# Performance work log

Hardware: AMD Instinct MI355X
Metric: run time of the kernel (lower is better)

## Reference

```python
import jax, jax.numpy as jnp
import numpy as np

N, E, G = 50000, 500000, 8
IN, HID, OUT, NC, H = 256, 128, 64, 10, 2
NPG = N // G  # nodes per graph
NEG_SLOPE = 0.2


def setup_inputs() -> dict:
    key = jax.random.key(0)
    ks = jax.random.split(key, 24)
    x = jax.random.normal(ks[0], (N, IN), jnp.float32)
    # edges constrained to stay within each graph, no self-loops
    src = jax.random.randint(ks[1], (E,), 0, N)
    base = (src // NPG) * NPG
    off = jax.random.randint(ks[2], (E,), 1, NPG)
    dst = base + (src - base + off) % NPG
    edge_index = jnp.stack([src, dst], axis=0).astype(jnp.int32)
    edge_attr = jax.random.uniform(ks[3], (E, 1), jnp.float32)
    batch = jnp.repeat(jnp.arange(G, dtype=jnp.int32), NPG)
    y = jax.random.randint(ks[4], (N,), 0, NC).astype(jnp.int32)

    s = 0.1
    p = {
        'W1': jax.random.normal(ks[5], (IN, H * HID), jnp.float32) * s,
        'att_src1': jax.random.normal(ks[6], (H, HID), jnp.float32) * s,
        'att_dst1': jax.random.normal(ks[7], (H, HID), jnp.float32) * s,
        'We1': jax.random.normal(ks[8], (1, H * HID), jnp.float32) * s,
        'att_edge1': jax.random.normal(ks[9], (H, HID), jnp.float32) * s,
        'b1': jnp.zeros((HID,), jnp.float32),
        'W2': jax.random.normal(ks[10], (HID, H * OUT), jnp.float32) * s,
        'att_src2': jax.random.normal(ks[11], (H, OUT), jnp.float32) * s,
        'att_dst2': jax.random.normal(ks[12], (H, OUT), jnp.float32) * s,
        'We2': jax.random.normal(ks[13], (1, H * OUT), jnp.float32) * s,
        'att_edge2': jax.random.normal(ks[14], (H, OUT), jnp.float32) * s,
        'b2': jnp.zeros((OUT,), jnp.float32),
        'Wc': jax.random.normal(ks[15], (OUT, NC), jnp.float32) * s,
        'bc': jnp.zeros((NC,), jnp.float32),
    }
    return dict(x=x, edge_index=edge_index, edge_attr=edge_attr, batch=batch, y=y, **p)


def _gat_layer(x, src, dst, eattr, W, a_src, a_dst, We, a_e, b, n_nodes, C):
    # PyG GATConv: heads=H, concat=False (mean over heads), edge_dim features.
    xp = (x @ W).reshape(n_nodes, H, C)                    # [N,H,C]
    al_s = jnp.einsum('nhc,hc->nh', xp, a_src)             # [N,H]
    al_d = jnp.einsum('nhc,hc->nh', xp, a_dst)
    ef = (eattr @ We).reshape(-1, H, C)                    # [E,H,C]
    al_e = jnp.einsum('ehc,hc->eh', ef, a_e)               # [E,H]
    alpha = jax.nn.leaky_relu(al_s[src] + al_d[dst] + al_e, NEG_SLOPE)
    # edge softmax grouped by destination (every dst has a self-loop -> no empty segs)
    m = jax.ops.segment_max(alpha, dst, num_segments=n_nodes)
    ex = jnp.exp(alpha - m[dst])
    denom = jax.ops.segment_sum(ex, dst, num_segments=n_nodes)
    w = ex / (denom[dst] + 1e-16)                          # [E,H]
    msg = xp[src] * w[:, :, None]                          # [E,H,C]
    out = jax.ops.segment_sum(msg, dst, num_segments=n_nodes)  # [N,H,C]
    return out.mean(axis=1) + b


def reference(x, edge_index, edge_attr, batch, y,
              W1, att_src1, att_dst1, We1, att_edge1, b1,
              W2, att_src2, att_dst2, We2, att_edge2, b2,
              Wc, bc):
    src, dst = edge_index[0], edge_index[1]
    # add self-loops; edge_attr fill = per-graph mean (as in the per-graph loop)
    g = batch[src]
    cnt = jax.ops.segment_sum(jnp.ones_like(edge_attr[:, 0]), g, num_segments=G)
    mean_attr = jax.ops.segment_sum(edge_attr, g, num_segments=G) / cnt[:, None]
    loop_attr = mean_attr[batch]                           # [N,1]
    ar = jnp.arange(N, dtype=src.dtype)
    src_a = jnp.concatenate([src, ar])
    dst_a = jnp.concatenate([dst, ar])
    ea = jnp.concatenate([edge_attr, loop_attr], axis=0)

    h = _gat_layer(x, src_a, dst_a, ea, W1, att_src1, att_dst1, We1, att_edge1, b1, N, HID)
    h = jax.nn.relu(h)
    h = _gat_layer(h, src_a, dst_a, ea, W2, att_src2, att_dst2, We2, att_edge2, b2, N, OUT)
    pred = h @ Wc + bc                                     # [N,NC]
    return pred, y
```

## Files before the change

kernel.cpp:

```cpp
#include <hip/hip_runtime.h>
#include <hip/hip_bf16.h>
#include <cstdint>
#include <cstddef>

#define N_NODES 50000
#define N_EDGES 500000
#define EA_EDGES 550000
#define NPG 6250
#define G_GRAPHS 8
#define IN_DIM 256
#define HID_DIM 128
#define OUT_DIM 64
#define NCLS 10
#define NEG_SLOPE 0.2f
#define M_PAD 50048

typedef __attribute__((ext_vector_type(8))) short short8v;
typedef __attribute__((ext_vector_type(4))) float f32x4;

__device__ __forceinline__ unsigned short f2bf(float f) {
  __hip_bfloat16 h = __float2bfloat16(f);
  unsigned short u;
  __builtin_memcpy(&u, &h, 2);
  return u;
}
__device__ __forceinline__ float bf2f(unsigned short u) {
  return __uint_as_float(((unsigned)u) << 16);
}

__device__ __forceinline__ void gl_lds16(const unsigned short* g, unsigned short* l) {
  __builtin_amdgcn_global_load_lds(
      (const __attribute__((address_space(1))) unsigned int*)(g),
      (__attribute__((address_space(3))) unsigned int*)(l),
      16, 0, 0);
}

__global__ void k_sums_degree(const int* __restrict__ src, const int* __restrict__ dst,
                              const float* __restrict__ eattr,
                              float* __restrict__ sums, float* __restrict__ cnts,
                              int* __restrict__ deg) {
  __shared__ float ls[G_GRAPHS], lc[G_GRAPHS];
  if (threadIdx.x < G_GRAPHS) { ls[threadIdx.x] = 0.f; lc[threadIdx.x] = 0.f; }
  __syncthreads();
  int stride = gridDim.x * blockDim.x;
  for (int e = blockIdx.x * blockDim.x + threadIdx.x; e < EA_EDGES; e += stride) {
    if (e < N_EDGES) {
      int g = src[e] / NPG;
      atomicAdd(&ls[g], eattr[e]);
      atomicAdd(&lc[g], 1.f);
      atomicAdd(&deg[dst[e]], 1);
    } else {
      atomicAdd(&deg[e - N_EDGES], 1);
    }
  }
  __syncthreads();
  if (threadIdx.x < G_GRAPHS) {
    atomicAdd(&sums[threadIdx.x], ls[threadIdx.x]);
    atomicAdd(&cnts[threadIdx.x], lc[threadIdx.x]);
  }
}

__global__ void k_prep(const float* __restrict__ sums, const float* __restrict__ cnts,
                       float* __restrict__ mean,
                       const float* __restrict__ We1, const float* __restrict__ ae1,
                       const float* __restrict__ We2, const float* __restrict__ ae2,
                       float* __restrict__ ce) {
  if (threadIdx.x == 0 && blockIdx.x == 0) {
    for (int g = 0; g < G_GRAPHS; ++g) mean[g] = sums[g] / cnts[g];
    for (int h = 0; h < 2; ++h) {
      float s = 0.f;
      for (int c = 0; c < HID_DIM; ++c) s += We1[h * HID_DIM + c] * ae1[h * HID_DIM + c];
      ce[h] = s;
    }
    for (int h = 0; h < 2; ++h) {
      float s = 0.f;
      for (int c = 0; c < OUT_DIM; ++c) s += We2[h * OUT_DIM + c] * ae2[h * OUT_DIM + c];
      ce[2 + h] = s;
    }
  }
}

__global__ void k_scan1(const int* __restrict__ deg, int* __restrict__ rowptr,
                        int* __restrict__ bsum, int n) {
  __shared__ int sm[1024];
  int tid = threadIdx.x;
  int i = blockIdx.x * 1024 + tid;
  int v = (i < n) ? deg[i] : 0;
  sm[tid] = v;
  __syncthreads();
  for (int off = 1; off < 1024; off <<= 1) {
    int t = (tid >= off) ? sm[tid - off] : 0;
    __syncthreads();
    if (tid >= off) sm[tid] += t;
    __syncthreads();
  }
  if (i < n) rowptr[i] = sm[tid] - v;
  if (tid == 1023) bsum[blockIdx.x] = sm[1023];
}

__global__ void k_scan2(int* __restrict__ bsum, int* __restrict__ rowptr, int nb, int n) {
  if (threadIdx.x == 0 && blockIdx.x == 0) {
    int run = 0;
    for (int i = 0; i < nb; ++i) { int v = bsum[i]; bsum[i] = run; run += v; }
    rowptr[n] = run;
  }
}

__global__ void k_scan3(int* __restrict__ rowptr, int* __restrict__ cursor,
                        const int* __restrict__ bsum, int n) {
  int i = blockIdx.x * blockDim.x + threadIdx.x;
  if (i < n) {
    int r = rowptr[i] + bsum[i >> 10];
    rowptr[i] = r;
    cursor[i] = r;
  }
}

__global__ void k_fill(const int* __restrict__ src, const int* __restrict__ dst,
                       const float* __restrict__ eattr, const float* __restrict__ mean,
                       int* __restrict__ cursor, int2* __restrict__ csr) {
  int e = blockIdx.x * blockDim.x + threadIdx.x;
  if (e >= EA_EDGES) return;
  int s, d; float a;
  if (e < N_EDGES) { s = src[e]; d = dst[e]; a = eattr[e]; }
  else { int i = e - N_EDGES; s = i; d = i; a = mean[i / NPG]; }
  int p = atomicAdd(&cursor[d], 1);
  csr[p] = make_int2(s, __float_as_int(a));
}

__global__ void k_cast_bf16(const float* __restrict__ in, unsigned short* __restrict__ out, int n8) {
  int i = blockIdx.x * blockDim.x + threadIdx.x;
  if (i >= n8) return;
  float4 a = *(const float4*)(in + (size_t)i * 8);
  float4 b = *(const float4*)(in + (size_t)i * 8 + 4);
  uint4 o;
  o.x = (unsigned)f2bf(a.x) | ((unsigned)f2bf(a.y) << 16);
  o.y = (unsigned)f2bf(a.z) | ((unsigned)f2bf(a.w) << 16);
  o.z = (unsigned)f2bf(b.x) | ((unsigned)f2bf(b.y) << 16);
  o.w = (unsigned)f2bf(b.z) | ((unsigned)f2bf(b.w) << 16);
  *(uint4*)(out + (size_t)i * 8) = o;
}

__global__ void k_cast_t(const float* __restrict__ W, unsigned short* __restrict__ Wt,
                         int K, int N) {
  int i = blockIdx.x * blockDim.x + threadIdx.x;
  if (i >= K * N) return;
  int k = i / N, n = i - k * N;
  Wt[(size_t)n * K + k] = f2bf(W[i]);
}

template <int K>
__global__ __launch_bounds__(256) void k_gemm_mfma(const unsigned short* __restrict__ A,
                                                   const unsigned short* __restrict__ Bt,
                                                   unsigned short* __restrict__ C,
                                                   int M, int Nout,
                                                   const float* __restrict__ a_src,
                                                   const float* __restrict__ a_dst,
                                                   float* __restrict__ als,
                                                   float* __restrict__ ald) {
  constexpr int BM = 128, BN = 128, BK = 64;
  constexpr int TSZ = BM * BK;
  __shared__ __attribute__((aligned(16))) unsigned short As[2 * TSZ];
  __shared__ __attribute__((aligned(16))) unsigned short Bs[2 * TSZ];
  const int tid = threadIdx.x;
  const int lane = tid & 63;
  const int wid = tid >> 6;
  const int wr = wid >> 1, wc = wid & 1;
  const int r0 = blockIdx.y * BM, c0 = blockIdx.x * BN;
  f32x4 acc[4][4] = {};

  const int srow = wid * 32 + (lane >> 3);
  const int schunk = (lane & 7) ^ (lane >> 3);
  const unsigned short* gA = A + (size_t)(r0 + srow) * K + schunk * 8;
  const unsigned short* gB = Bt + (size_t)(c0 + srow) * K + schunk * 8;

  auto stage = [&](int buf, int k0) {
    unsigned short* Ab = As + buf * TSZ + wid * 2048;
    unsigned short* Bb = Bs + buf * TSZ + wid * 2048;
#pragma unroll
    for (int i = 0; i < 4; ++i) {
      gl_lds16(gA + (size_t)(i * 8) * K + k0, Ab + i * 512);
      gl_lds16(gB + (size_t)(i * 8) * K + k0, Bb + i * 512);
    }
  };

  constexpr int NT = K / BK;
  int cur = 0;
  stage(0, 0);
#pragma unroll
  for (int t = 0; t < NT; ++t) {
    __syncthreads();
    if (t + 1 < NT) stage(cur ^ 1, (t + 1) * BK);
    const char* Ab = (const char*)(As + cur * TSZ);
    const char* Bb = (const char*)(Bs + cur * TSZ);
#pragma unroll
    for (int ks = 0; ks < 2; ++ks) {
      short8v a[4], b[4];
#pragma unroll
      for (int mi = 0; mi < 4; ++mi) {
        int row = wr * 64 + mi * 16 + (lane & 15);
        int boff = (row * 128 + ks * 64 + (lane >> 4) * 16) ^ ((row & 7) << 4);
        a[mi] = *(const short8v*)(Ab + boff);
      }
#pragma unroll
      for (int ni = 0; ni < 4; ++ni) {
        int row = wc * 64 + ni * 16 + (lane & 15);
        int boff = (row * 128 + ks * 64 + (lane >> 4) * 16) ^ ((row & 7) << 4);
        b[ni] = *(const short8v*)(Bb + boff);
      }
#pragma unroll
      for (int mi = 0; mi < 4; ++mi)
#pragma unroll
        for (int ni = 0; ni < 4; ++ni)
          acc[mi][ni] = __builtin_amdgcn_mfma_f32_16x16x32_bf16(a[mi], b[ni], acc[mi][ni], 0, 0, 0);
    }
    cur ^= 1;
  }

#pragma unroll
  for (int mi = 0; mi < 4; ++mi) {
#pragma unroll
    for (int r = 0; r < 4; ++r) {
      int row = r0 + wr * 64 + mi * 16 + (lane >> 4) * 4 + r;
      if (row < M) {
#pragma unroll
        for (int ni = 0; ni < 4; ++ni) {
          int col = c0 + wc * 64 + ni * 16 + (lane & 15);
          C[(size_t)row * Nout + col] = f2bf(acc[mi][ni][r]);
        }
      }
    }
  }

  {
    int headc = (c0 + wc * 64) / (Nout >> 1);
    float asv[4], adv[4];
#pragma unroll
    for (int ni = 0; ni < 4; ++ni) {
      int col = c0 + wc * 64 + ni * 16 + (lane & 15);
      asv[ni] = a_src[col];
      adv[ni] = a_dst[col];
    }
#pragma unroll
    for (int mi = 0; mi < 4; ++mi) {
#pragma unroll
      for (int r = 0; r < 4; ++r) {
        float ps = 0.f, pd = 0.f;
#pragma unroll
        for (int ni = 0; ni < 4; ++ni) {
          ps += acc[mi][ni][r] * asv[ni];
          pd += acc[mi][ni][r] * adv[ni];
        }
#pragma unroll
        for (int off = 1; off < 16; off <<= 1) {
          ps += __shfl_xor(ps, off);
          pd += __shfl_xor(pd, off);
        }
        int row = r0 + wr * 64 + mi * 16 + (lane >> 4) * 4 + r;
        if ((lane & 15) == 0 && row < M) {
          atomicAdd(&als[2 * row + headc], ps);
          atomicAdd(&ald[2 * row + headc], pd);
        }
      }
    }
  }
}

template <int C, bool RELU, bool BF16OUT>
__global__ void k_aggregate(const unsigned short* __restrict__ xp,
                            const float* __restrict__ als, const float* __restrict__ ald,
                            const int* __restrict__ rowptr, const int2* __restrict__ csr,
                            const float* __restrict__ ce,
                            const float* __restrict__ bias, void* __restrict__ outv) {
  constexpr int TC = 2 * C;
  constexpr int VPL = TC / 64;
  int lane = threadIdx.x & 63;
  int wid = threadIdx.x >> 6;
  int local = (blockIdx.x >> 3) * 4 + wid;
  if (local >= NPG) return;
  int node = (blockIdx.x & 7) * NPG + local;
  int p0 = rowptr[node], p1 = rowptr[node + 1];
  int deg = p1 - p0;
  int half = lane >> 5;
  int sub = lane & 31;
  float ald_m = ald[2 * node + half];
  float ce_m = ce[half];
  float m = -1e30f, den = 0.f;
  float acc[VPL];
#pragma unroll
  for (int k = 0; k < VPL; ++k) acc[k] = 0.f;

  for (int base = 0; base < deg; base += 32) {
    int nE = min(32, deg - base);
    float a = -1e30f;
    int s = 0;
    float w = 0.f;
    if (sub < nE) {
      int2 md = csr[p0 + base + sub];
      s = md.x;
      float ea = __int_as_float(md.y);
      float l = als[2 * s + half] + ald_m + ce_m * ea;
      a = (l > 0.f) ? l : NEG_SLOPE * l;
    }
    float cm = a;
#pragma unroll
    for (int off = 1; off < 32; off <<= 1) cm = fmaxf(cm, __shfl_xor(cm, off));
    float nm = fmaxf(m, cm);
    float cs = __expf(m - nm);
    m = nm;
    if (sub < nE) w = __expf(a - m);
    float ws = w;
#pragma unroll
    for (int off = 1; off < 32; off <<= 1) ws += __shfl_xor(ws, off);
    den = den * cs + ws;
#pragma unroll
    for (int k = 0; k < VPL; ++k) acc[k] *= cs;
    for (int e0 = 0; e0 < nE; e0 += 8) {
      int se[8]; float wh[8];
#pragma unroll
      for (int j = 0; j < 8; ++j) {
        int e = e0 + j;
        se[j] = __shfl(s, e);
        wh[j] = __shfl(w, e | (lane & 32));
      }
      if (VPL == 4) {
        ushort4 u[8];
#pragma unroll
        for (int j = 0; j < 8; ++j)
          u[j] = *(const ushort4*)(xp + (size_t)se[j] * TC + lane * VPL);
#pragma unroll
        for (int j = 0; j < 8; ++j) {
          acc[0] += wh[j] * bf2f(u[j].x);
          acc[1] += wh[j] * bf2f(u[j].y);
          acc[2] += wh[j] * bf2f(u[j].z);
          acc[3] += wh[j] * bf2f(u[j].w);
        }
      } else {
        ushort2 u[8];
#pragma unroll
        for (int j = 0; j < 8; ++j)
          u[j] = *(const ushort2*)(xp + (size_t)se[j] * TC + lane * VPL);
#pragma unroll
        for (int j = 0; j < 8; ++j) {
          acc[0] += wh[j] * bf2f(u[j].x);
          acc[1] += wh[j] * bf2f(u[j].y);
        }
      }
    }
  }

  float deni = 1.f / (den + 1e-16f);
  float t[VPL];
#pragma unroll
  for (int k = 0; k < VPL; ++k) {
    t[k] = acc[k] * deni;
    t[k] += __shfl_xor(t[k], 32);
  }
  if (lane < 32) {
    int c = lane * VPL;
    float v[VPL];
#pragma unroll
    for (int k = 0; k < VPL; ++k) {
      v[k] = 0.5f * t[k] + bias[c + k];
      if (RELU) v[k] = fmaxf(v[k], 0.f);
    }
    if (BF16OUT) {
      unsigned short* o = (unsigned short*)outv + (size_t)node * C + c;
      if (VPL == 4) {
        ushort4 u;
        u.x = f2bf(v[0]); u.y = f2bf(v[1]); u.z = f2bf(v[2]); u.w = f2bf(v[3]);
        *(ushort4*)o = u;
      } else {
        ushort2 u; u.x = f2bf(v[0]); u.y = f2bf(v[1]);
        *(ushort2*)o = u;
      }
    } else {
      float* o = (float*)outv + (size_t)node * C + c;
#pragma unroll
      for (int k = 0; k < VPL; ++k) o[k] = v[k];
    }
  }
}

__global__ void k_classifier(const float* __restrict__ h2, const float* __restrict__ Wc,
                             const float* __restrict__ bc, const int* __restrict__ y,
                             float* __restrict__ out) {
  __shared__ float wcs[OUT_DIM * NCLS];
  __shared__ float bcs[NCLS];
  for (int i = threadIdx.x; i < OUT_DIM * NCLS; i += blockDim.x) wcs[i] = Wc[i];
  if (threadIdx.x < NCLS) bcs[threadIdx.x] = bc[threadIdx.x];
  __syncthreads();
  int n = blockIdx.x * blockDim.x + threadIdx.x;
  if (n >= N_NODES) return;
  float acc[NCLS];
#pragma unroll
  for (int j = 0; j < NCLS; ++j) acc[j] = bcs[j];
  for (int k = 0; k < OUT_DIM; ++k) {
    float v = h2[(size_t)n * OUT_DIM + k];
#pragma unroll
    for (int j = 0; j < NCLS; ++j) acc[j] += v * wcs[k * NCLS + j];
  }
#pragma unroll
  for (int j = 0; j < NCLS; ++j) out[(size_t)n * NCLS + j] = acc[j];
  out[(size_t)N_NODES * NCLS + n] = (float)y[n];
}

extern "C" void kernel_launch(void* const* d_in, const int* in_sizes, int n_in,
                              void* d_out, int out_size, void* d_ws, size_t ws_size,
                              hipStream_t stream) {
  const float* x     = (const float*)d_in[0];
  const int*   ei    = (const int*)d_in[1];
  const float* eattr = (const float*)d_in[2];
  const int*   y     = (const int*)d_in[4];
  const float* W1  = (const float*)d_in[5];
  const float* as1 = (const float*)d_in[6];
  const float* ad1 = (const float*)d_in[7];
  const float* We1 = (const float*)d_in[8];
  const float* ae1 = (const float*)d_in[9];
  const float* b1  = (const float*)d_in[10];
  const float* W2  = (const float*)d_in[11];
  const float* as2 = (const float*)d_in[12];
  const float* ad2 = (const float*)d_in[13];
  const float* We2 = (const float*)d_in[14];
  const float* ae2 = (const float*)d_in[15];
  const float* b2  = (const float*)d_in[16];
  const float* Wc  = (const float*)d_in[17];
  const float* bc  = (const float*)d_in[18];
  float* out = (float*)d_out;

  const int* src = ei;
  const int* dst = ei + N_EDGES;

  char* wsb = (char*)d_ws;
  size_t o = 0;
  auto alloc = [&](size_t bytes) { size_t r = o; o = (o + bytes + 255) & ~(size_t)255; return r; };
  size_t o_sums   = alloc(G_GRAPHS * 4);
  size_t o_cnts   = alloc(G_GRAPHS * 4);
  size_t o_mean   = alloc(G_GRAPHS * 4);
  size_t o_ce     = alloc(4 * 4);
  size_t o_bsum   = alloc(64 * 4);
  size_t o_deg    = alloc((size_t)N_NODES * 4);
  size_t o_rowptr = alloc((size_t)(N_NODES + 1) * 4);
  size_t o_cursor = alloc((size_t)N_NODES * 4);
  size_t o_csr    = alloc((size_t)EA_EDGES * 8);
  size_t o_xb     = alloc((size_t)M_PAD * IN_DIM * 2);
  size_t o_wt1    = alloc((size_t)IN_DIM * 256 * 2);
  size_t o_wt2    = alloc((size_t)HID_DIM * 128 * 2);
  size_t o_xp     = alloc((size_t)N_NODES * 256 * 2);
  size_t o_h1b    = alloc((size_t)M_PAD * HID_DIM * 2);
  size_t o_h2     = alloc((size_t)N_NODES * OUT_DIM * 4);
  size_t o_als    = alloc((size_t)N_NODES * 2 * 4);
  size_t o_ald    = alloc((size_t)N_NODES * 2 * 4);
  (void)ws_size;

  float* sums   = (float*)(wsb + o_sums);
  float* cnts   = (float*)(wsb + o_cnts);
  float* mean   = (float*)(wsb + o_mean);
  float* ce     = (float*)(wsb + o_ce);
  int*   bsum   = (int*)(wsb + o_bsum);
  int*   deg    = (int*)(wsb + o_deg);
  int*   rowptr = (int*)(wsb + o_rowptr);
  int*   cursor = (int*)(wsb + o_cursor);
  int2*  csr    = (int2*)(wsb + o_csr);
  unsigned short* xb  = (unsigned short*)(wsb + o_xb);
  unsigned short* wt1 = (unsigned short*)(wsb + o_wt1);
  unsigned short* wt2 = (unsigned short*)(wsb + o_wt2);
  unsigned short* xp  = (unsigned short*)(wsb + o_xp);
  unsigned short* h1b = (unsigned short*)(wsb + o_h1b);
  float* h2     = (float*)(wsb + o_h2);
  float* als    = (float*)(wsb + o_als);
  float* ald    = (float*)(wsb + o_ald);
  size_t alsald_bytes = (o_ald - o_als) + (size_t)N_NODES * 2 * 4;

  hipMemsetAsync(sums, 0, G_GRAPHS * 4 * 2, stream);
  hipMemsetAsync(deg, 0, (size_t)N_NODES * 4, stream);

  k_cast_bf16<<<(N_NODES * IN_DIM / 8 + 255) / 256, 256, 0, stream>>>(x, xb, N_NODES * IN_DIM / 8);
  k_cast_t<<<(IN_DIM * 256 + 255) / 256, 256, 0, stream>>>(W1, wt1, IN_DIM, 256);
  k_cast_t<<<(HID_DIM * 128 + 255) / 256, 256, 0, stream>>>(W2, wt2, HID_DIM, 128);

  k_sums_degree<<<512, 256, 0, stream>>>(src, dst, eattr, sums, cnts, deg);
  k_prep<<<1, 64, 0, stream>>>(sums, cnts, mean, We1, ae1, We2, ae2, ce);

  int eaBlocks = (EA_EDGES + 255) / 256;
  int nScanBlocks = (N_NODES + 1023) / 1024;
  k_scan1<<<nScanBlocks, 1024, 0, stream>>>(deg, rowptr, bsum, N_NODES);
  k_scan2<<<1, 64, 0, stream>>>(bsum, rowptr, nScanBlocks, N_NODES);
  k_scan3<<<(N_NODES + 255) / 256, 256, 0, stream>>>(rowptr, cursor, bsum, N_NODES);
  k_fill<<<eaBlocks, 256, 0, stream>>>(src, dst, eattr, mean, cursor, csr);

  int aggBlocks = G_GRAPHS * ((NPG + 3) / 4);

  hipMemsetAsync(als, 0, alsald_bytes, stream);
  {
    dim3 grid(256 / 128, M_PAD / 128);
    k_gemm_mfma<IN_DIM><<<grid, 256, 0, stream>>>(xb, wt1, xp, N_NODES, 256,
                                                  as1, ad1, als, ald);
  }
  k_aggregate<HID_DIM, true, true><<<aggBlocks, 256, 0, stream>>>(
      xp, als, ald, rowptr, csr, ce, b1, h1b);

  hipMemsetAsync(als, 0, alsald_bytes, stream);
  {
    dim3 grid(128 / 128, M_PAD / 128);
    k_gemm_mfma<HID_DIM><<<grid, 256, 0, stream>>>(h1b, wt2, xp, N_NODES, 128,
                                                   as2, ad2, als, ald);
  }
  k_aggregate<OUT_DIM, false, false><<<aggBlocks, 256, 0, stream>>>(
      xp, als, ald, rowptr, csr, ce + 2, b2, h2);

  k_classifier<<<(N_NODES + 255) / 256, 256, 0, stream>>>(h2, Wc, bc, y, out);
}
```

Measured before the change: 333.1 us.

## Parallelize prep/scan kernels, merge casts, single-buffer GEMM LDS, readlane in aggregation

The serial single-thread k_prep and k_scan2 now use wavefront shuffle reductions and scans. The three cast kernels are merged into one launch. The GEMM drops LDS double buffering for a single buffer plus an extra barrier, with launch bounds raised for occupancy. The aggregation loop replaces per-edge shuffles with readlane and skips tail edges past the count. Together these cut launch and serial overhead, but the GEMM now loses overlap between global loads and MFMA work.

Result: faster. 314.6 us (-5.6%).

```diff
diff --git a/kernel.cpp b/kernel.cpp
--- a/kernel.cpp
+++ b/kernel.cpp
@@ -26,6 +26,9 @@
 }
 __device__ __forceinline__ float bf2f(unsigned short u) {
   return __uint_as_float(((unsigned)u) << 16);
+}
+__device__ __forceinline__ float readlane_f(float v, int l) {
+  return __int_as_float(__builtin_amdgcn_readlane(__float_as_int(v), l));
 }
 
 __device__ __forceinline__ void gl_lds16(const unsigned short* g, unsigned short* l) {
@@ -65,19 +68,16 @@
                        const float* __restrict__ We1, const float* __restrict__ ae1,
                        const float* __restrict__ We2, const float* __restrict__ ae2,
                        float* __restrict__ ce) {
-  if (threadIdx.x == 0 && blockIdx.x == 0) {
-    for (int g = 0; g < G_GRAPHS; ++g) mean[g] = sums[g] / cnts[g];
-    for (int h = 0; h < 2; ++h) {
-      float s = 0.f;
-      for (int c = 0; c < HID_DIM; ++c) s += We1[h * HID_DIM + c] * ae1[h * HID_DIM + c];
-      ce[h] = s;
-    }
-    for (int h = 0; h < 2; ++h) {
-      float s = 0.f;
-      for (int c = 0; c < OUT_DIM; ++c) s += We2[h * OUT_DIM + c] * ae2[h * OUT_DIM + c];
-      ce[2 + h] = s;
-    }
-  }
+  int wid = threadIdx.x >> 6, lane = threadIdx.x & 63;
+  float p;
+  if (wid == 0)      p = We1[lane] * ae1[lane] + We1[64 + lane] * ae1[64 + lane];
+  else if (wid == 1) p = We1[128 + lane] * ae1[128 + lane] + We1[192 + lane] * ae1[192 + lane];
+  else if (wid == 2) p = We2[lane] * ae2[lane];
+  else               p = We2[64 + lane] * ae2[64 + lane];
+#pragma unroll
+  for (int off = 1; off < 64; off <<= 1) p += __shfl_xor(p, off);
+  if (lane == 0) ce[wid] = p;
+  if (threadIdx.x < G_GRAPHS) mean[threadIdx.x] = sums[threadIdx.x] / cnts[threadIdx.x];
 }
 
 __global__ void k_scan1(const int* __restrict__ deg, int* __restrict__ rowptr,
@@ -99,11 +99,17 @@
 }
 
 __global__ void k_scan2(int* __restrict__ bsum, int* __restrict__ rowptr, int nb, int n) {
-  if (threadIdx.x == 0 && blockIdx.x == 0) {
-    int run = 0;
-    for (int i = 0; i < nb; ++i) { int v = bsum[i]; bsum[i] = run; run += v; }
-    rowptr[n] = run;
-  }
+  int lane = threadIdx.x & 63;
+  int v = (lane < nb) ? bsum[lane] : 0;
+  int x = v;
+#pragma unroll
+  for (int off = 1; off < 64; off <<= 1) {
+    int t = __shfl_up(x, off);
+    if (lane >= off) x += t;
+  }
+  int total = __shfl(x, nb - 1);
+  if (lane < nb) bsum[lane] = x - v;
+  if (lane == 0) rowptr[n] = total;
 }
 
 __global__ void k_scan3(int* __restrict__ rowptr, int* __restrict__ cursor,
@@ -128,40 +134,44 @@
   csr[p] = make_int2(s, __float_as_int(a));
 }
 
-__global__ void k_cast_bf16(const float* __restrict__ in, unsigned short* __restrict__ out, int n8) {
+#define NX_CHUNKS (N_NODES * IN_DIM / 8)
+__global__ void k_cast_all(const float* __restrict__ x, unsigned short* __restrict__ xb,
+                           const float* __restrict__ W1, unsigned short* __restrict__ wt1,
+                           const float* __restrict__ W2, unsigned short* __restrict__ wt2) {
   int i = blockIdx.x * blockDim.x + threadIdx.x;
-  if (i >= n8) return;
-  float4 a = *(const float4*)(in + (size_t)i * 8);
-  float4 b = *(const float4*)(in + (size_t)i * 8 + 4);
-  uint4 o;
-  o.x = (unsigned)f2bf(a.x) | ((unsigned)f2bf(a.y) << 16);
-  o.y = (unsigned)f2bf(a.z) | ((unsigned)f2bf(a.w) << 16);
-  o.z = (unsigned)f2bf(b.x) | ((unsigned)f2bf(b.y) << 16);
-  o.w = (unsigned)f2bf(b.z) | ((unsigned)f2bf(b.w) << 16);
-  *(uint4*)(out + (size_t)i * 8) = o;
-}
-
-__global__ void k_cast_t(const float* __restrict__ W, unsigned short* __restrict__ Wt,
-                         int K, int N) {
-  int i = blockIdx.x * blockDim.x + threadIdx.x;
-  if (i >= K * N) return;
-  int k = i / N, n = i - k * N;
-  Wt[(size_t)n * K + k] = f2bf(W[i]);
+  if (i < NX_CHUNKS) {
+    float4 a = *(const float4*)(x + (size_t)i * 8);
+    float4 b = *(const float4*)(x + (size_t)i * 8 + 4);
+    uint4 o;
+    o.x = (unsigned)f2bf(a.x) | ((unsigned)f2bf(a.y) << 16);
+    o.y = (unsigned)f2bf(a.z) | ((unsigned)f2bf(a.w) << 16);
+    o.z = (unsigned)f2bf(b.x) | ((unsigned)f2bf(b.y) << 16);
+    o.w = (unsigned)f2bf(b.z) | ((unsigned)f2bf(b.w) << 16);
+    *(uint4*)(xb + (size_t)i * 8) = o;
+  } else if (i < NX_CHUNKS + 256 * 256) {
+    int j = i - NX_CHUNKS;
+    int k = j >> 8, nn = j & 255;
+    wt1[nn * 256 + k] = f2bf(W1[j]);
+  } else if (i < NX_CHUNKS + 256 * 256 + 128 * 128) {
+    int j = i - NX_CHUNKS - 256 * 256;
+    int k = j >> 7, nn = j & 127;
+    wt2[nn * 128 + k] = f2bf(W2[j]);
+  }
 }
 
 template <int K>
-__global__ __launch_bounds__(256) void k_gemm_mfma(const unsigned short* __restrict__ A,
-                                                   const unsigned short* __restrict__ Bt,
-                                                   unsigned short* __restrict__ C,
-                                                   int M, int Nout,
-                                                   const float* __restrict__ a_src,
-                                                   const float* __restrict__ a_dst,
-                                                   float* __restrict__ als,
-                                                   float* __restrict__ ald) {
+__global__ __launch_bounds__(256, 4) void k_gemm_mfma(const unsigned short* __restrict__ A,
+                                                      const unsigned short* __restrict__ Bt,
+                                                      unsigned short* __restrict__ C,
+                                                      int M, int Nout,
+                                                      const float* __restrict__ a_src,
+                                                      const float* __restrict__ a_dst,
+                                                      float* __restrict__ als,
+                                                      float* __restrict__ ald) {
   constexpr int BM = 128, BN = 128, BK = 64;
   constexpr int TSZ = BM * BK;
-  __shared__ __attribute__((aligned(16))) unsigned short As[2 * TSZ];
-  __shared__ __attribute__((aligned(16))) unsigned short Bs[2 * TSZ];
+  __shared__ __attribute__((aligned(16))) unsigned short As[TSZ];
+  __shared__ __attribute__((aligned(16))) unsigned short Bs[TSZ];
   const int tid = threadIdx.x;
   const int lane = tid & 63;
   const int wid = tid >> 6;
@@ -174,9 +184,9 @@
   const unsigned short* gA = A + (size_t)(r0 + srow) * K + schunk * 8;
   const unsigned short* gB = Bt + (size_t)(c0 + srow) * K + schunk * 8;
 
-  auto stage = [&](int buf, int k0) {
-    unsigned short* Ab = As + buf * TSZ + wid * 2048;
-    unsigned short* Bb = Bs + buf * TSZ + wid * 2048;
+  auto stage = [&](int k0) {
+    unsigned short* Ab = As + wid * 2048;
+    unsigned short* Bb = Bs + wid * 2048;
 #pragma unroll
     for (int i = 0; i < 4; ++i) {
       gl_lds16(gA + (size_t)(i * 8) * K + k0, Ab + i * 512);
@@ -185,14 +195,12 @@
   };
 
   constexpr int NT = K / BK;
-  int cur = 0;
-  stage(0, 0);
+  stage(0);
 #pragma unroll
   for (int t = 0; t < NT; ++t) {
     __syncthreads();
-    if (t + 1 < NT) stage(cur ^ 1, (t + 1) * BK);
-    const char* Ab = (const char*)(As + cur * TSZ);
-    const char* Bb = (const char*)(Bs + cur * TSZ);
+    const char* Ab = (const char*)As;
+    const char* Bb = (const char*)Bs;
 #pragma unroll
     for (int ks = 0; ks < 2; ++ks) {
       short8v a[4], b[4];
@@ -214,7 +222,10 @@
         for (int ni = 0; ni < 4; ++ni)
           acc[mi][ni] = __builtin_amdgcn_mfma_f32_16x16x32_bf16(a[mi], b[ni], acc[mi][ni], 0, 0, 0);
     }
-    cur ^= 1;
+    if (t + 1 < NT) {
+      __syncthreads();
+      stage((t + 1) * BK);
+    }
   }
 
 #pragma unroll
@@ -283,6 +294,7 @@
   int deg = p1 - p0;
   int half = lane >> 5;
   int sub = lane & 31;
+  bool lowhalf = (lane < 32);
   float ald_m = ald[2 * node + half];
   float ce_m = ce[half];
   float m = -1e30f, den = 0.f;
@@ -316,34 +328,47 @@
 #pragma unroll
     for (int k = 0; k < VPL; ++k) acc[k] *= cs;
     for (int e0 = 0; e0 < nE; e0 += 8) {
-      int se[8]; float wh[8];
-#pragma unroll
-      for (int j = 0; j < 8; ++j) {
-        int e = e0 + j;
-        se[j] = __shfl(s, e);
-        wh[j] = __shfl(w, e | (lane & 32));
-      }
+      int cnt = nE - e0;
+      float wh_[8];
       if (VPL == 4) {
-        ushort4 u[8];
-#pragma unroll
-        for (int j = 0; j < 8; ++j)
-          u[j] = *(const ushort4*)(xp + (size_t)se[j] * TC + lane * VPL);
+        ushort4 u_[8];
 #pragma unroll
         for (int j = 0; j < 8; ++j) {
-          acc[0] += wh[j] * bf2f(u[j].x);
-          acc[1] += wh[j] * bf2f(u[j].y);
-          acc[2] += wh[j] * bf2f(u[j].z);
-          acc[3] += wh[j] * bf2f(u[j].w);
+          if (j < cnt) {
+            int se = __builtin_amdgcn_readlane(s, e0 + j);
+            float w0 = readlane_f(w, e0 + j);
+            float w1 = readlane_f(w, e0 + j + 32);
+            wh_[j] = lowhalf ? w0 : w1;
+            u_[j] = *(const ushort4*)(xp + (size_t)se * TC + lane * VPL);
+          }
+        }
+#pragma unroll
+        for (int j = 0; j < 8; ++j) {
+          if (j < cnt) {
+            acc[0] += wh_[j] * bf2f(u_[j].x);
+            acc[1] += wh_[j] * bf2f(u_[j].y);
+            acc[2] += wh_[j] * bf2f(u_[j].z);
+            acc[3] += wh_[j] * bf2f(u_[j].w);
+          }
         }
       } else {
-        ushort2 u[8];
-#pragma unroll
-        for (int j = 0; j < 8; ++j)
-          u[j] = *(const ushort2*)(xp + (size_t)se[j] * TC + lane * VPL);
+        ushort2 u_[8];
 #pragma unroll
         for (int j = 0; j < 8; ++j) {
-          acc[0] += wh[j] * bf2f(u[j].x);
-          acc[1] += wh[j] * bf2f(u[j].y);
+          if (j < cnt) {
+            int se = __builtin_amdgcn_readlane(s, e0 + j);
+            float w0 = readlane_f(w, e0 + j);
+            float w1 = readlane_f(w, e0 + j + 32);
+            wh_[j] = lowhalf ? w0 : w1;
+            u_[j] = *(const ushort2*)(xp + (size_t)se * TC + lane * VPL);
+          }
+        }
+#pragma unroll
+        for (int j = 0; j < 8; ++j) {
+          if (j < cnt) {
+            acc[0] += wh_[j] * bf2f(u_[j].x);
+            acc[1] += wh_[j] * bf2f(u_[j].y);
+          }
         }
       }
     }
@@ -475,12 +500,13 @@
   hipMemsetAsync(sums, 0, G_GRAPHS * 4 * 2, stream);
   hipMemsetAsync(deg, 0, (size_t)N_NODES * 4, stream);
 
-  k_cast_bf16<<<(N_NODES * IN_DIM / 8 + 255) / 256, 256, 0, stream>>>(x, xb, N_NODES * IN_DIM / 8);
-  k_cast_t<<<(IN_DIM * 256 + 255) / 256, 256, 0, stream>>>(W1, wt1, IN_DIM, 256);
-  k_cast_t<<<(HID_DIM * 128 + 255) / 256, 256, 0, stream>>>(W2, wt2, HID_DIM, 128);
+  {
+    int total = NX_CHUNKS + 256 * 256 + 128 * 128;
+    k_cast_all<<<(total + 255) / 256, 256, 0, stream>>>(x, xb, W1, wt1, W2, wt2);
+  }
 
   k_sums_degree<<<512, 256, 0, stream>>>(src, dst, eattr, sums, cnts, deg);
-  k_prep<<<1, 64, 0, stream>>>(sums, cnts, mean, We1, ae1, We2, ae2, ce);
+  k_prep<<<1, 256, 0, stream>>>(sums, cnts, mean, We1, ae1, We2, ae2, ce);
 
   int eaBlocks = (EA_EDGES + 255) / 256;
   int nScanBlocks = (N_NODES + 1023) / 1024;
```
